# Performance work log

Hardware: AMD Instinct MI355X
Metric: run time of the kernel (lower is better)

The kernel has to match this reference:

```python
import jax, jax.numpy as jnp
import numpy as np

D_MODEL = 768
NUM_HEADS = 12
HEAD_DIM = D_MODEL // NUM_HEADS
LN_EPS = 1e-5
MASK_NEG = -1000000.0


def setup_inputs() -> dict:
    key = jax.random.key(0)
    ks = jax.random.split(key, 10)
    B, L, S = 2, 2048, 2048
    s = 1.0 / np.sqrt(D_MODEL)
    return {
        "q": jax.random.normal(ks[0], (B, L, D_MODEL), jnp.float32),
        "k": jax.random.normal(ks[1], (B, S, D_MODEL), jnp.float32),
        "v": jax.random.normal(ks[2], (B, S, D_MODEL), jnp.float32),
        "attention_mask": jnp.ones((B, S), jnp.int32),
        "Wq": jax.random.normal(ks[3], (D_MODEL, D_MODEL), jnp.float32) * s,
        "Wk": jax.random.normal(ks[4], (D_MODEL, D_MODEL), jnp.float32) * s,
        "Wv": jax.random.normal(ks[5], (D_MODEL, D_MODEL), jnp.float32) * s,
        "W": jax.random.normal(ks[6], (D_MODEL, D_MODEL), jnp.float32) * s,
        "b": jnp.zeros((D_MODEL,), jnp.float32),
        "gamma": jnp.ones((D_MODEL,), jnp.float32),
        "beta": jnp.zeros((D_MODEL,), jnp.float32),
    }


def reference(q, k, v, attention_mask, Wq, Wk, Wv, W, b, gamma, beta):
    B, L, D = q.shape
    S = k.shape[1]
    H, hd = NUM_HEADS, HEAD_DIM
    # projections (torch Linear: x @ W^T), split heads -> (B,H,L,hd)
    Q = (q @ Wq.T).reshape(B, L, H, hd).transpose(0, 2, 1, 3)
    K = (k @ Wk.T).reshape(B, S, H, hd).transpose(0, 2, 1, 3)
    V = (v @ Wv.T).reshape(B, S, H, hd).transpose(0, 2, 1, 3)
    # scores (B,H,L,S) with additive key-padding mask
    scores = jnp.einsum("bhld,bhsd->bhls", Q, K) / np.sqrt(hd)
    mask_score = (1.0 - attention_mask.astype(q.dtype))[:, None, None, :] * MASK_NEG
    att = jax.nn.softmax(scores + mask_score, axis=-1)  # dropout p=0 (eval)
    # attend, merge heads, output projection (with bias)
    O = jnp.einsum("bhls,bhsd->bhld", att, V).transpose(0, 2, 1, 3).reshape(B, L, D)
    O = O @ W.T + b  # state dropout p=0 (eval)
    # residual + LayerNorm
    x = q + O
    mu = jnp.mean(x, axis=-1, keepdims=True)
    var = jnp.mean(jnp.square(x - mu), axis=-1, keepdims=True)
    return (x - mu) * jax.lax.rsqrt(var + LN_EPS) * gamma + beta
```

## Files before the change

kernel.cpp:

```cpp
#include <hip/hip_runtime.h>
#include <hip/hip_bf16.h>
#include <math.h>


typedef unsigned short u16;
typedef unsigned int   u32;
typedef __bf16 bf16x8 __attribute__((ext_vector_type(8)));
typedef float  f32x4  __attribute__((ext_vector_type(4)));

#define DM   768
#define MR   4096
#define WSZ  589824

#define LOG2E 1.44269504089f
#define SM_C  15.0f
#define K1    (0.125f * LOG2E)

__device__ inline u16 bfbits(float f) {
    union { __bf16 b; u16 u; } x; x.b = (__bf16)f; return x.u;
}

__device__ inline uint4 cvt8(const float* src) {
    const float4* p = reinterpret_cast<const float4*>(src);
    float4 a = p[0], b = p[1];
    union { __bf16 h[8]; uint4 v; } u;
    u.h[0] = (__bf16)a.x; u.h[1] = (__bf16)a.y; u.h[2] = (__bf16)a.z; u.h[3] = (__bf16)a.w;
    u.h[4] = (__bf16)b.x; u.h[5] = (__bf16)b.y; u.h[6] = (__bf16)b.z; u.h[7] = (__bf16)b.w;
    return u.v;
}

__device__ inline uint4 cvt8v(float4 a, float4 b) {
    union { __bf16 h[8]; uint4 v; } u;
    u.h[0] = (__bf16)a.x; u.h[1] = (__bf16)a.y; u.h[2] = (__bf16)a.z; u.h[3] = (__bf16)a.w;
    u.h[4] = (__bf16)b.x; u.h[5] = (__bf16)b.y; u.h[6] = (__bf16)b.z; u.h[7] = (__bf16)b.w;
    return u.v;
}

__global__ __launch_bounds__(256) void wcvt(
    const float* __restrict__ w0, const float* __restrict__ w1,
    const float* __restrict__ w2, const float* __restrict__ w3,
    u16* __restrict__ dst)
{
    const float* src = (blockIdx.y == 0) ? w0 : (blockIdx.y == 1) ? w1
                     : (blockIdx.y == 2) ? w2 : w3;
    size_t idx = ((size_t)blockIdx.x * 256 + threadIdx.x) * 8;
    *reinterpret_cast<uint4*>(&dst[(size_t)blockIdx.y * WSZ + idx]) = cvt8(&src[idx]);
}

__global__ __launch_bounds__(256, 2) void gemm_qkv(
    const float* __restrict__ xq, const float* __restrict__ xk, const float* __restrict__ xv,
    const u16* __restrict__ Wb4,
    u16* __restrict__ oq, u16* __restrict__ ok, u16* __restrict__ ov)
{
    const int mode = blockIdx.z;
    const float* X = (mode == 0) ? xq : (mode == 1) ? xk : xv;
    const u16* Wb  = Wb4 + (size_t)mode * WSZ;
    u16* out       = (mode == 0) ? oq : (mode == 1) ? ok : ov;

    __shared__ __attribute__((aligned(16))) u16 As[2][64][72];
    __shared__ __attribute__((aligned(16))) u16 Bs[2][64][72];

    const int tid  = threadIdx.x;
    const int lane = tid & 63;
    const int w    = tid >> 6;
    const int wm   = (w >> 1) * 32;
    const int wn   = (w & 1) * 32;
    const int quad = lane >> 4;
    const int l16  = lane & 15;
    const int tm   = blockIdx.x * 64;
    const int tn   = blockIdx.y * 64;

    const int row0 = tid >> 3,         col0 = (tid & 7) * 8;
    const int row1 = (tid + 256) >> 3, col1 = ((tid + 256) & 7) * 8;

    const float* a0p = &X[(size_t)(tm + row0) * 768 + col0];
    const float* a1p = &X[(size_t)(tm + row1) * 768 + col1];
    const u16*   b0p = &Wb[(size_t)(tn + row0) * 768 + col0];
    const u16*   b1p = &Wb[(size_t)(tn + row1) * 768 + col1];

    f32x4 acc[2][2] = {};

    {
        *reinterpret_cast<uint4*>(&As[0][row0][col0]) = cvt8(a0p);
        *reinterpret_cast<uint4*>(&As[0][row1][col1]) = cvt8(a1p);
        *reinterpret_cast<uint4*>(&Bs[0][row0][col0]) = *reinterpret_cast<const uint4*>(b0p);
        *reinterpret_cast<uint4*>(&Bs[0][row1][col1]) = *reinterpret_cast<const uint4*>(b1p);
    }

    for (int kt = 0; kt < 12; kt++) {
        const int cur = kt & 1;
        __syncthreads();

        float4 af0a, af0b, af1a, af1b; uint4 bt0, bt1;
        if (kt < 11) {
            const int ko = (kt + 1) * 64;
            af0a = *reinterpret_cast<const float4*>(a0p + ko);
            af0b = *reinterpret_cast<const float4*>(a0p + ko + 4);
            af1a = *reinterpret_cast<const float4*>(a1p + ko);
            af1b = *reinterpret_cast<const float4*>(a1p + ko + 4);
            bt0  = *reinterpret_cast<const uint4*>(b0p + ko);
            bt1  = *reinterpret_cast<const uint4*>(b1p + ko);
        }

        #pragma unroll
        for (int kk = 0; kk < 2; kk++) {
            bf16x8 a0 = *reinterpret_cast<const bf16x8*>(&As[cur][wm + l16     ][kk*32 + quad*8]);
            bf16x8 a1 = *reinterpret_cast<const bf16x8*>(&As[cur][wm + 16 + l16][kk*32 + quad*8]);
            bf16x8 b0 = *reinterpret_cast<const bf16x8*>(&Bs[cur][wn + l16     ][kk*32 + quad*8]);
            bf16x8 b1 = *reinterpret_cast<const bf16x8*>(&Bs[cur][wn + 16 + l16][kk*32 + quad*8]);
            acc[0][0] = __builtin_amdgcn_mfma_f32_16x16x32_bf16(a0, b0, acc[0][0], 0, 0, 0);
            acc[0][1] = __builtin_amdgcn_mfma_f32_16x16x32_bf16(a0, b1, acc[0][1], 0, 0, 0);
            acc[1][0] = __builtin_amdgcn_mfma_f32_16x16x32_bf16(a1, b0, acc[1][0], 0, 0, 0);
            acc[1][1] = __builtin_amdgcn_mfma_f32_16x16x32_bf16(a1, b1, acc[1][1], 0, 0, 0);
        }

        if (kt < 11) {
            const int nxt = cur ^ 1;
            *reinterpret_cast<uint4*>(&As[nxt][row0][col0]) = cvt8v(af0a, af0b);
            *reinterpret_cast<uint4*>(&As[nxt][row1][col1]) = cvt8v(af1a, af1b);
            *reinterpret_cast<uint4*>(&Bs[nxt][row0][col0]) = bt0;
            *reinterpret_cast<uint4*>(&Bs[nxt][row1][col1]) = bt1;
        }
    }

    #pragma unroll
    for (int i = 0; i < 2; i++)
        #pragma unroll
        for (int j = 0; j < 2; j++)
            #pragma unroll
            for (int r = 0; r < 4; r++) {
                int gm = tm + wm + i * 16 + quad * 4 + r;
                int gn = tn + wn + j * 16 + l16;
                int b = gm >> 11, l = gm & 2047;
                int h = gn >> 6,  d = gn & 63;
                u16 bv = bfbits(acc[i][j][r]);
                if (mode == 2)
                    out[((size_t)(b * 12 + h) * 64 + d) * 2048 + l] = bv;
                else
                    out[((size_t)(b * 12 + h) * 2048 + l) * 64 + d] = bv;
            }
}

__global__ __launch_bounds__(256, 2) void gemm_out(
    const u16* __restrict__ Oa, const u16* __restrict__ Wb,
    const float* __restrict__ bias, const float* __restrict__ resid,
    float* __restrict__ Xb)
{
    __shared__ __attribute__((aligned(16))) u16 As[2][64][72];
    __shared__ __attribute__((aligned(16))) u16 Bs[2][64][72];

    const int tid  = threadIdx.x;
    const int lane = tid & 63;
    const int w    = tid >> 6;
    const int wm   = (w >> 1) * 32;
    const int wn   = (w & 1) * 32;
    const int quad = lane >> 4;
    const int l16  = lane & 15;
    const int tm   = blockIdx.x * 64;
    const int tn   = blockIdx.y * 64;

    const int row0 = tid >> 3,         col0 = (tid & 7) * 8;
    const int row1 = (tid + 256) >> 3, col1 = ((tid + 256) & 7) * 8;

    const u16* a0p = &Oa[(size_t)(tm + row0) * 768 + col0];
    const u16* a1p = &Oa[(size_t)(tm + row1) * 768 + col1];
    const u16* b0p = &Wb[(size_t)(tn + row0) * 768 + col0];
    const u16* b1p = &Wb[(size_t)(tn + row1) * 768 + col1];

    f32x4 acc[2][2] = {};

    {
        *reinterpret_cast<uint4*>(&As[0][row0][col0]) = *reinterpret_cast<const uint4*>(a0p);
        *reinterpret_cast<uint4*>(&As[0][row1][col1]) = *reinterpret_cast<const uint4*>(a1p);
        *reinterpret_cast<uint4*>(&Bs[0][row0][col0]) = *reinterpret_cast<const uint4*>(b0p);
        *reinterpret_cast<uint4*>(&Bs[0][row1][col1]) = *reinterpret_cast<const uint4*>(b1p);
    }

    for (int kt = 0; kt < 12; kt++) {
        const int cur = kt & 1;
        __syncthreads();

        uint4 at0, at1, bt0, bt1;
        if (kt < 11) {
            const int ko = (kt + 1) * 64;
            at0 = *reinterpret_cast<const uint4*>(a0p + ko);
            at1 = *reinterpret_cast<const uint4*>(a1p + ko);
            bt0 = *reinterpret_cast<const uint4*>(b0p + ko);
            bt1 = *reinterpret_cast<const uint4*>(b1p + ko);
        }

        #pragma unroll
        for (int kk = 0; kk < 2; kk++) {
            bf16x8 a0 = *reinterpret_cast<const bf16x8*>(&As[cur][wm + l16     ][kk*32 + quad*8]);
            bf16x8 a1 = *reinterpret_cast<const bf16x8*>(&As[cur][wm + 16 + l16][kk*32 + quad*8]);
            bf16x8 b0 = *reinterpret_cast<const bf16x8*>(&Bs[cur][wn + l16     ][kk*32 + quad*8]);
            bf16x8 b1 = *reinterpret_cast<const bf16x8*>(&Bs[cur][wn + 16 + l16][kk*32 + quad*8]);
            acc[0][0] = __builtin_amdgcn_mfma_f32_16x16x32_bf16(a0, b0, acc[0][0], 0, 0, 0);
            acc[0][1] = __builtin_amdgcn_mfma_f32_16x16x32_bf16(a0, b1, acc[0][1], 0, 0, 0);
            acc[1][0] = __builtin_amdgcn_mfma_f32_16x16x32_bf16(a1, b0, acc[1][0], 0, 0, 0);
            acc[1][1] = __builtin_amdgcn_mfma_f32_16x16x32_bf16(a1, b1, acc[1][1], 0, 0, 0);
        }

        if (kt < 11) {
            const int nxt = cur ^ 1;
            *reinterpret_cast<uint4*>(&As[nxt][row0][col0]) = at0;
            *reinterpret_cast<uint4*>(&As[nxt][row1][col1]) = at1;
            *reinterpret_cast<uint4*>(&Bs[nxt][row0][col0]) = bt0;
            *reinterpret_cast<uint4*>(&Bs[nxt][row1][col1]) = bt1;
        }
    }

    #pragma unroll
    for (int i = 0; i < 2; i++)
        #pragma unroll
        for (int j = 0; j < 2; j++)
            #pragma unroll
            for (int r = 0; r < 4; r++) {
                int gm = tm + wm + i * 16 + quad * 4 + r;
                int gn = tn + wn + j * 16 + l16;
                Xb[(size_t)gm * 768 + gn] = acc[i][j][r] + bias[gn] + resid[(size_t)gm * 768 + gn];
            }
}

__global__ __launch_bounds__(256, 3) void attn(
    const u16* __restrict__ Qp, const u16* __restrict__ Kp, const u16* __restrict__ Vt,
    const int* __restrict__ amask, u16* __restrict__ Oatt)
{
    __shared__ __attribute__((aligned(16))) unsigned char smem[4 * 64 * 40 * 2 + 2048 * 4];
    u16 (*Ps)[64][40] = reinterpret_cast<u16(*)[64][40]>(smem);
    float* maskC = reinterpret_cast<float*>(smem + 20480);
    float (*Obuf)[72] = reinterpret_cast<float(*)[72]>(smem);

    const int tid  = threadIdx.x;
    const int lane = tid & 63;
    const int w    = tid >> 6;
    const int quad = lane >> 4;
    const int l16  = lane & 15;
    const int qt = blockIdx.x;
    const int h  = blockIdx.y;
    const int b  = blockIdx.z;

    #pragma unroll
    for (int i = 0; i < 8; i++) {
        int s = tid + i * 256;
        maskC[s] = amask[b * 2048 + s] ? (-SM_C * LOG2E) : -2.0e6f;
    }
    __syncthreads();

    const u16* Qbase = Qp + ((size_t)(b * 12 + h) * 2048 + qt * 64) * 64;
    const u16* Kb2   = Kp + (size_t)(b * 12 + h) * 2048 * 64 + (size_t)w * 32 * 64;
    const u16* Vb2   = Vt + (size_t)(b * 12 + h) * 64 * 2048 + (size_t)w * 32;

    bf16x8 qfrag[4][2];
    #pragma unroll
    for (int qb = 0; qb < 4; qb++)
        #pragma unroll
        for (int kk = 0; kk < 2; kk++)
            qfrag[qb][kk] = *reinterpret_cast<const bf16x8*>(
                &Qbase[(qb * 16 + l16) * 64 + kk * 32 + quad * 8]);

    bf16x8 onesf = {};
    if (l16 == 0) {
        #pragma unroll
        for (int i = 0; i < 8; i++) onesf[i] = (__bf16)1.0f;
    }

    f32x4 oacc[4][4] = {};
    f32x4 sacc[4]    = {};

    for (int st = 0; st < 16; st++) {
        bf16x8 kf[2][2], vf[4];
        #pragma unroll
        for (int ct = 0; ct < 2; ct++)
            #pragma unroll
            for (int kk = 0; kk < 2; kk++)
                kf[ct][kk] = *reinterpret_cast<const bf16x8*>(
                    &Kb2[(size_t)(st * 128 + ct * 16 + l16) * 64 + kk * 32 + quad * 8]);
        #pragma unroll
        for (int cd = 0; cd < 4; cd++)
            vf[cd] = *reinterpret_cast<const bf16x8*>(
                &Vb2[(size_t)(cd * 16 + l16) * 2048 + st * 128 + quad * 8]);

        #pragma unroll
        for (int qb = 0; qb < 4; qb++)
            #pragma unroll
            for (int ct = 0; ct < 2; ct++) {
                f32x4 s = {};
                s = __builtin_amdgcn_mfma_f32_16x16x32_bf16(kf[ct][0], qfrag[qb][0], s, 0, 0, 0);
                s = __builtin_amdgcn_mfma_f32_16x16x32_bf16(kf[ct][1], qfrag[qb][1], s, 0, 0, 0);
                f32x4 cc = *reinterpret_cast<const f32x4*>(
                    &maskC[st * 128 + w * 32 + ct * 16 + quad * 4]);
                union { u16 h[4]; uint2 v2; } pk;
                #pragma unroll
                for (int r = 0; r < 4; r++)
                    pk.h[r] = bfbits(__builtin_amdgcn_exp2f(__builtin_fmaf(s[r], K1, cc[r])));
                *reinterpret_cast<uint2*>(&Ps[w][qb * 16 + l16][ct * 16 + quad * 4]) = pk.v2;
            }

        bf16x8 pf[4];
        #pragma unroll
        for (int qb = 0; qb < 4; qb++)
            pf[qb] = *reinterpret_cast<const bf16x8*>(&Ps[w][qb * 16 + l16][quad * 8]);
        #pragma unroll
        for (int qb = 0; qb < 4; qb++)
            sacc[qb] = __builtin_amdgcn_mfma_f32_16x16x32_bf16(pf[qb], onesf, sacc[qb], 0, 0, 0);
        #pragma unroll
        for (int qb = 0; qb < 4; qb++)
            #pragma unroll
            for (int cd = 0; cd < 4; cd++)
                oacc[qb][cd] = __builtin_amdgcn_mfma_f32_16x16x32_bf16(pf[qb], vf[cd], oacc[qb][cd], 0, 0, 0);
    }

    __syncthreads();
    for (int wv = 0; wv < 4; wv++) {
        if (w == wv) {
            #pragma unroll
            for (int qb = 0; qb < 4; qb++) {
                #pragma unroll
                for (int cd = 0; cd < 4; cd++)
                    #pragma unroll
                    for (int r = 0; r < 4; r++) {
                        float* cell = &Obuf[qb * 16 + quad * 4 + r][cd * 16 + l16];
                        if (wv == 0) *cell = oacc[qb][cd][r];
                        else         *cell += oacc[qb][cd][r];
                    }
                if (l16 == 0) {
                    #pragma unroll
                    for (int r = 0; r < 4; r++) {
                        float* cell = &Obuf[qb * 16 + quad * 4 + r][64];
                        if (wv == 0) *cell = sacc[qb][r];
                        else         *cell += sacc[qb][r];
                    }
                }
            }
        }
        __syncthreads();
    }

    #pragma unroll
    for (int g = 0; g < 4; g++) {
        int unit = tid + g * 256;
        int row = unit >> 4;
        int c4  = (unit & 15) * 4;
        float rinv = 1.0f / Obuf[row][64];
        union { u16 h[4]; uint2 v; } o;
        #pragma unroll
        for (int j = 0; j < 4; j++)
            o.h[j] = bfbits(Obuf[row][c4 + j] * rinv);
        *reinterpret_cast<uint2*>(
            &Oatt[(size_t)(b * 2048 + qt * 64 + row) * 768 + h * 64 + c4]) = o.v;
    }
}

__global__ __launch_bounds__(256) void ln_kernel(
    float* __restrict__ X, const float* __restrict__ gamma,
    const float* __restrict__ beta)
{
    const int row = blockIdx.x;
    const int tid = threadIdx.x;
    float* xr = X + (size_t)row * 768;

    float v[3], s = 0.f, s2 = 0.f;
    #pragma unroll
    for (int i = 0; i < 3; i++) {
        v[i] = xr[tid + i * 256];
        s += v[i];
        s2 += v[i] * v[i];
    }
    #pragma unroll
    for (int off = 32; off >= 1; off >>= 1) {
        s  += __shfl_xor(s,  off, 64);
        s2 += __shfl_xor(s2, off, 64);
    }
    __shared__ float rs[4], rs2[4];
    int w = tid >> 6, lane = tid & 63;
    if (lane == 0) { rs[w] = s; rs2[w] = s2; }
    __syncthreads();
    s  = rs[0] + rs[1] + rs[2] + rs[3];
    s2 = rs2[0] + rs2[1] + rs2[2] + rs2[3];
    float mu = s * (1.0f / 768.0f);
    float var = s2 * (1.0f / 768.0f) - mu * mu;
    float rstd = rsqrtf(var + 1e-5f);
    #pragma unroll
    for (int i = 0; i < 3; i++) {
        int c = tid + i * 256;
        xr[c] = (v[i] - mu) * rstd * gamma[c] + beta[c];
    }
}

extern "C" void kernel_launch(void* const* d_in, const int* in_sizes, int n_in,
                              void* d_out, int out_size, void* d_ws, size_t ws_size,
                              hipStream_t stream)
{
    const float* q   = (const float*)d_in[0];
    const float* k   = (const float*)d_in[1];
    const float* v   = (const float*)d_in[2];
    const int*   am  = (const int*)d_in[3];
    const float* Wq  = (const float*)d_in[4];
    const float* Wk  = (const float*)d_in[5];
    const float* Wv  = (const float*)d_in[6];
    const float* W   = (const float*)d_in[7];
    const float* bb  = (const float*)d_in[8];
    const float* gam = (const float*)d_in[9];
    const float* bet = (const float*)d_in[10];

    u16* Wb4 = (u16*)d_ws;
    u16* Qp  = Wb4 + (size_t)4 * WSZ;
    u16* Kp  = Qp + (size_t)MR * DM;
    u16* Vt  = Kp + (size_t)MR * DM;
    u16* Oa  = Vt + (size_t)MR * DM;
    float* Xb = (float*)d_out;

    wcvt<<<dim3(288, 4), 256, 0, stream>>>(Wq, Wk, Wv, W, Wb4);
    gemm_qkv<<<dim3(64, 12, 3), 256, 0, stream>>>(q, k, v, Wb4, Qp, Kp, Vt);
    attn<<<dim3(32, 12, 2), 256, 0, stream>>>(Qp, Kp, Vt, am, Oa);
    gemm_out<<<dim3(64, 12), 256, 0, stream>>>(Oa, Wb4 + (size_t)3 * WSZ, bb, q, Xb);
    ln_kernel<<<4096, 256, 0, stream>>>(Xb, gam, bet);
}
```

Baseline: 218.1 us.

## Shrink attention query tile, prefetch K/V fragments, precompute mask globally

The attention kernel now handles 32 query rows per block instead of 64, doubling the grid and raising the occupancy hint from 3 to 4 blocks per CU. K and V fragments for the next key tile are loaded as soon as the current ones are consumed, a one-step software prefetch. The key-padding mask is precomputed once into a float buffer by an extra block in the weight-conversion kernel, which removes per-block LDS mask setup. The cross-wave reduction of partial outputs now uses two LDS buffers in two stages instead of four serial rounds. The trade-off is that each block redoes the full K/V stream for half as many queries, doubling K/V load traffic.

```diff
diff --git a/kernel.cpp b/kernel.cpp
--- a/kernel.cpp
+++ b/kernel.cpp
@@ -39,8 +39,20 @@
 __global__ __launch_bounds__(256) void wcvt(
     const float* __restrict__ w0, const float* __restrict__ w1,
     const float* __restrict__ w2, const float* __restrict__ w3,
-    u16* __restrict__ dst)
-{
+    const int* __restrict__ am, u16* __restrict__ dst,
+    float* __restrict__ maskF)
+{
+    if (blockIdx.x == 288) {
+        int i = (blockIdx.y * 256 + threadIdx.x) * 4;
+        int4 m = *reinterpret_cast<const int4*>(&am[i]);
+        float4 o;
+        o.x = m.x ? (-SM_C * LOG2E) : -2.0e6f;
+        o.y = m.y ? (-SM_C * LOG2E) : -2.0e6f;
+        o.z = m.z ? (-SM_C * LOG2E) : -2.0e6f;
+        o.w = m.w ? (-SM_C * LOG2E) : -2.0e6f;
+        *reinterpret_cast<float4*>(&maskF[i]) = o;
+        return;
+    }
     const float* src = (blockIdx.y == 0) ? w0 : (blockIdx.y == 1) ? w1
                      : (blockIdx.y == 2) ? w2 : w3;
     size_t idx = ((size_t)blockIdx.x * 256 + threadIdx.x) * 8;
@@ -222,14 +234,14 @@
             }
 }
 
-__global__ __launch_bounds__(256, 3) void attn(
+__global__ __launch_bounds__(256, 4) void attn(
     const u16* __restrict__ Qp, const u16* __restrict__ Kp, const u16* __restrict__ Vt,
-    const int* __restrict__ amask, u16* __restrict__ Oatt)
-{
-    __shared__ __attribute__((aligned(16))) unsigned char smem[4 * 64 * 40 * 2 + 2048 * 4];
-    u16 (*Ps)[64][40] = reinterpret_cast<u16(*)[64][40]>(smem);
-    float* maskC = reinterpret_cast<float*>(smem + 20480);
-    float (*Obuf)[72] = reinterpret_cast<float(*)[72]>(smem);
+    const float* __restrict__ maskF, u16* __restrict__ Oatt)
+{
+    __shared__ __attribute__((aligned(16))) unsigned char smem[2 * 32 * 68 * 4];
+    u16 (*Ps)[32][40] = reinterpret_cast<u16(*)[32][40]>(smem);
+    float (*O0)[68] = reinterpret_cast<float(*)[68]>(smem);
+    float (*O1)[68] = reinterpret_cast<float(*)[68]>(smem + 32 * 68 * 4);
 
     const int tid  = threadIdx.x;
     const int lane = tid & 63;
@@ -240,20 +252,14 @@
     const int h  = blockIdx.y;
     const int b  = blockIdx.z;
 
-    #pragma unroll
-    for (int i = 0; i < 8; i++) {
-        int s = tid + i * 256;
-        maskC[s] = amask[b * 2048 + s] ? (-SM_C * LOG2E) : -2.0e6f;
-    }
-    __syncthreads();
-
-    const u16* Qbase = Qp + ((size_t)(b * 12 + h) * 2048 + qt * 64) * 64;
+    const u16* Qbase = Qp + ((size_t)(b * 12 + h) * 2048 + qt * 32) * 64;
     const u16* Kb2   = Kp + (size_t)(b * 12 + h) * 2048 * 64 + (size_t)w * 32 * 64;
     const u16* Vb2   = Vt + (size_t)(b * 12 + h) * 64 * 2048 + (size_t)w * 32;
-
-    bf16x8 qfrag[4][2];
-    #pragma unroll
-    for (int qb = 0; qb < 4; qb++)
+    const float* mB  = maskF + b * 2048 + w * 32;
+
+    bf16x8 qfrag[2][2];
+    #pragma unroll
+    for (int qb = 0; qb < 2; qb++)
         #pragma unroll
         for (int kk = 0; kk < 2; kk++)
             qfrag[qb][kk] = *reinterpret_cast<const bf16x8*>(
@@ -265,90 +271,120 @@
         for (int i = 0; i < 8; i++) onesf[i] = (__bf16)1.0f;
     }
 
-    f32x4 oacc[4][4] = {};
-    f32x4 sacc[4]    = {};
+    f32x4 oacc[2][4] = {};
+    f32x4 sacc[2]    = {};
+
+    bf16x8 kf[2][2], vf[4];
+    #pragma unroll
+    for (int ct = 0; ct < 2; ct++)
+        #pragma unroll
+        for (int kk = 0; kk < 2; kk++)
+            kf[ct][kk] = *reinterpret_cast<const bf16x8*>(
+                &Kb2[(size_t)(ct * 16 + l16) * 64 + kk * 32 + quad * 8]);
+    #pragma unroll
+    for (int cd = 0; cd < 4; cd++)
+        vf[cd] = *reinterpret_cast<const bf16x8*>(
+            &Vb2[(size_t)(cd * 16 + l16) * 2048 + quad * 8]);
 
     for (int st = 0; st < 16; st++) {
-        bf16x8 kf[2][2], vf[4];
-        #pragma unroll
-        for (int ct = 0; ct < 2; ct++)
-            #pragma unroll
-            for (int kk = 0; kk < 2; kk++)
-                kf[ct][kk] = *reinterpret_cast<const bf16x8*>(
-                    &Kb2[(size_t)(st * 128 + ct * 16 + l16) * 64 + kk * 32 + quad * 8]);
-        #pragma unroll
-        for (int cd = 0; cd < 4; cd++)
-            vf[cd] = *reinterpret_cast<const bf16x8*>(
-                &Vb2[(size_t)(cd * 16 + l16) * 2048 + st * 128 + quad * 8]);
-
-        #pragma unroll
-        for (int qb = 0; qb < 4; qb++)
-            #pragma unroll
-            for (int ct = 0; ct < 2; ct++) {
+        const int stn = (st + 1) & 15;
+
+        #pragma unroll
+        for (int ct = 0; ct < 2; ct++) {
+            f32x4 sv[2];
+            #pragma unroll
+            for (int qb = 0; qb < 2; qb++) {
                 f32x4 s = {};
                 s = __builtin_amdgcn_mfma_f32_16x16x32_bf16(kf[ct][0], qfrag[qb][0], s, 0, 0, 0);
                 s = __builtin_amdgcn_mfma_f32_16x16x32_bf16(kf[ct][1], qfrag[qb][1], s, 0, 0, 0);
-                f32x4 cc = *reinterpret_cast<const f32x4*>(
-                    &maskC[st * 128 + w * 32 + ct * 16 + quad * 4]);
+                sv[qb] = s;
+            }
+            #pragma unroll
+            for (int kk = 0; kk < 2; kk++)
+                kf[ct][kk] = *reinterpret_cast<const bf16x8*>(
+                    &Kb2[(size_t)(stn * 128 + ct * 16 + l16) * 64 + kk * 32 + quad * 8]);
+
+            f32x4 cc = *reinterpret_cast<const f32x4*>(&mB[st * 128 + ct * 16 + quad * 4]);
+            #pragma unroll
+            for (int qb = 0; qb < 2; qb++) {
                 union { u16 h[4]; uint2 v2; } pk;
                 #pragma unroll
                 for (int r = 0; r < 4; r++)
-                    pk.h[r] = bfbits(__builtin_amdgcn_exp2f(__builtin_fmaf(s[r], K1, cc[r])));
+                    pk.h[r] = bfbits(__builtin_amdgcn_exp2f(__builtin_fmaf(sv[qb][r], K1, cc[r])));
                 *reinterpret_cast<uint2*>(&Ps[w][qb * 16 + l16][ct * 16 + quad * 4]) = pk.v2;
             }
-
-        bf16x8 pf[4];
-        #pragma unroll
-        for (int qb = 0; qb < 4; qb++)
+        }
+
+        bf16x8 pf[2];
+        #pragma unroll
+        for (int qb = 0; qb < 2; qb++)
             pf[qb] = *reinterpret_cast<const bf16x8*>(&Ps[w][qb * 16 + l16][quad * 8]);
         #pragma unroll
-        for (int qb = 0; qb < 4; qb++)
+        for (int qb = 0; qb < 2; qb++)
             sacc[qb] = __builtin_amdgcn_mfma_f32_16x16x32_bf16(pf[qb], onesf, sacc[qb], 0, 0, 0);
         #pragma unroll
-        for (int qb = 0; qb < 4; qb++)
+        for (int qb = 0; qb < 2; qb++)
             #pragma unroll
             for (int cd = 0; cd < 4; cd++)
                 oacc[qb][cd] = __builtin_amdgcn_mfma_f32_16x16x32_bf16(pf[qb], vf[cd], oacc[qb][cd], 0, 0, 0);
+
+        #pragma unroll
+        for (int cd = 0; cd < 4; cd++)
+            vf[cd] = *reinterpret_cast<const bf16x8*>(
+                &Vb2[(size_t)(cd * 16 + l16) * 2048 + stn * 128 + quad * 8]);
     }
 
     __syncthreads();
-    for (int wv = 0; wv < 4; wv++) {
-        if (w == wv) {
-            #pragma unroll
-            for (int qb = 0; qb < 4; qb++) {
+    float (*Ob)[68] = (w & 1) ? O1 : O0;
+    if (w >= 2) {
+        #pragma unroll
+        for (int qb = 0; qb < 2; qb++) {
+            #pragma unroll
+            for (int cd = 0; cd < 4; cd++)
                 #pragma unroll
-                for (int cd = 0; cd < 4; cd++)
-                    #pragma unroll
-                    for (int r = 0; r < 4; r++) {
-                        float* cell = &Obuf[qb * 16 + quad * 4 + r][cd * 16 + l16];
-                        if (wv == 0) *cell = oacc[qb][cd][r];
-                        else         *cell += oacc[qb][cd][r];
-                    }
-                if (l16 == 0) {
-                    #pragma unroll
-                    for (int r = 0; r < 4; r++) {
-                        float* cell = &Obuf[qb * 16 + quad * 4 + r][64];
-                        if (wv == 0) *cell = sacc[qb][r];
-                        else         *cell += sacc[qb][r];
-                    }
+                for (int r = 0; r < 4; r++)
+                    Ob[qb * 16 + quad * 4 + r][cd * 16 + l16] = oacc[qb][cd][r];
+            if (l16 == 0) {
+                #pragma unroll
+                for (int r = 0; r < 4; r++)
+                    Ob[qb * 16 + quad * 4 + r][64] = sacc[qb][r];
+            }
+        }
+    }
+    __syncthreads();
+    if (w < 2) {
+        #pragma unroll
+        for (int qb = 0; qb < 2; qb++) {
+            #pragma unroll
+            for (int cd = 0; cd < 4; cd++)
+                #pragma unroll
+                for (int r = 0; r < 4; r++) {
+                    float* c = &Ob[qb * 16 + quad * 4 + r][cd * 16 + l16];
+                    *c += oacc[qb][cd][r];
                 }
-            }
-        }
-        __syncthreads();
-    }
-
-    #pragma unroll
-    for (int g = 0; g < 4; g++) {
+            if (l16 == 0) {
+                #pragma unroll
+                for (int r = 0; r < 4; r++) {
+                    float* c = &Ob[qb * 16 + quad * 4 + r][64];
+                    *c += sacc[qb][r];
+                }
+            }
+        }
+    }
+    __syncthreads();
+
+    #pragma unroll
+    for (int g = 0; g < 2; g++) {
         int unit = tid + g * 256;
         int row = unit >> 4;
         int c4  = (unit & 15) * 4;
-        float rinv = 1.0f / Obuf[row][64];
+        float rinv = 1.0f / (O0[row][64] + O1[row][64]);
         union { u16 h[4]; uint2 v; } o;
         #pragma unroll
         for (int j = 0; j < 4; j++)
-            o.h[j] = bfbits(Obuf[row][c4 + j] * rinv);
+            o.h[j] = bfbits((O0[row][c4 + j] + O1[row][c4 + j]) * rinv);
         *reinterpret_cast<uint2*>(
-            &Oatt[(size_t)(b * 2048 + qt * 64 + row) * 768 + h * 64 + c4]) = o.v;
+            &Oatt[(size_t)(b * 2048 + qt * 32 + row) * 768 + h * 64 + c4]) = o.v;
     }
 }
 
@@ -409,11 +445,12 @@
     u16* Kp  = Qp + (size_t)MR * DM;
     u16* Vt  = Kp + (size_t)MR * DM;
     u16* Oa  = Vt + (size_t)MR * DM;
+    float* maskF = (float*)(Oa + (size_t)MR * DM);
     float* Xb = (float*)d_out;
 
-    wcvt<<<dim3(288, 4), 256, 0, stream>>>(Wq, Wk, Wv, W, Wb4);
+    wcvt<<<dim3(289, 4), 256, 0, stream>>>(Wq, Wk, Wv, W, am, Wb4, maskF);
     gemm_qkv<<<dim3(64, 12, 3), 256, 0, stream>>>(q, k, v, Wb4, Qp, Kp, Vt);
-    attn<<<dim3(32, 12, 2), 256, 0, stream>>>(Qp, Kp, Vt, am, Oa);
+    attn<<<dim3(64, 12, 2), 256, 0, stream>>>(Qp, Kp, Vt, maskF, Oa);
     gemm_out<<<dim3(64, 12), 256, 0, stream>>>(Oa, Wb4 + (size_t)3 * WSZ, bb, q, Xb);
     ln_kernel<<<4096, 256, 0, stream>>>(Xb, gam, bet);
 }
```

Measured after the change: 261.8 us. +20.1%, slower.

## Prefetch K/V fragments across attention steps, precompute mask, remap blocks

Applied to the files above, without the earlier changes.

Converts the attention key-padding mask to float once in the weight-conversion kernel and reads it from global memory, which drops the per-block shared-memory mask setup and its barrier and shrinks LDS use. K and V fragments for the next step are loaded during the current step so global-load latency overlaps the MFMA and exp work, and s_setprio raises wave priority around the MFMA bursts. The grid is flattened to 1D and remapped so groups of 8 consecutive blocks cover different head/batch pairs, which changes how K/V traffic spreads across L2 and cache partitions. The extra prefetch registers may reduce occupancy, and the last iteration prefetches wrapped data it never uses.

```diff
diff --git a/kernel.cpp b/kernel.cpp
--- a/kernel.cpp
+++ b/kernel.cpp
@@ -39,8 +39,20 @@
 __global__ __launch_bounds__(256) void wcvt(
     const float* __restrict__ w0, const float* __restrict__ w1,
     const float* __restrict__ w2, const float* __restrict__ w3,
-    u16* __restrict__ dst)
-{
+    const int* __restrict__ am, u16* __restrict__ dst,
+    float* __restrict__ maskF)
+{
+    if (blockIdx.x == 288) {
+        int i = (blockIdx.y * 256 + threadIdx.x) * 4;
+        int4 m = *reinterpret_cast<const int4*>(&am[i]);
+        float4 o;
+        o.x = m.x ? (-SM_C * LOG2E) : -2.0e6f;
+        o.y = m.y ? (-SM_C * LOG2E) : -2.0e6f;
+        o.z = m.z ? (-SM_C * LOG2E) : -2.0e6f;
+        o.w = m.w ? (-SM_C * LOG2E) : -2.0e6f;
+        *reinterpret_cast<float4*>(&maskF[i]) = o;
+        return;
+    }
     const float* src = (blockIdx.y == 0) ? w0 : (blockIdx.y == 1) ? w1
                      : (blockIdx.y == 2) ? w2 : w3;
     size_t idx = ((size_t)blockIdx.x * 256 + threadIdx.x) * 8;
@@ -224,32 +236,30 @@
 
 __global__ __launch_bounds__(256, 3) void attn(
     const u16* __restrict__ Qp, const u16* __restrict__ Kp, const u16* __restrict__ Vt,
-    const int* __restrict__ amask, u16* __restrict__ Oatt)
-{
-    __shared__ __attribute__((aligned(16))) unsigned char smem[4 * 64 * 40 * 2 + 2048 * 4];
+    const float* __restrict__ maskF, u16* __restrict__ Oatt)
+{
+    __shared__ __attribute__((aligned(16))) unsigned char smem[4 * 64 * 40 * 2];
     u16 (*Ps)[64][40] = reinterpret_cast<u16(*)[64][40]>(smem);
-    float* maskC = reinterpret_cast<float*>(smem + 20480);
-    float (*Obuf)[72] = reinterpret_cast<float(*)[72]>(smem);
+    float (*Obuf)[68] = reinterpret_cast<float(*)[68]>(smem);
 
     const int tid  = threadIdx.x;
     const int lane = tid & 63;
     const int w    = tid >> 6;
     const int quad = lane >> 4;
     const int l16  = lane & 15;
-    const int qt = blockIdx.x;
-    const int h  = blockIdx.y;
-    const int b  = blockIdx.z;
-
-    #pragma unroll
-    for (int i = 0; i < 8; i++) {
-        int s = tid + i * 256;
-        maskC[s] = amask[b * 2048 + s] ? (-SM_C * LOG2E) : -2.0e6f;
-    }
-    __syncthreads();
+
+    const int bi  = blockIdx.x;
+    const int c   = bi & 7;
+    const int k8  = bi >> 3;
+    const int qt  = k8 & 31;
+    const int hc  = c + 8 * (k8 >> 5);
+    const int h   = hc % 12;
+    const int b   = hc / 12;
 
     const u16* Qbase = Qp + ((size_t)(b * 12 + h) * 2048 + qt * 64) * 64;
     const u16* Kb2   = Kp + (size_t)(b * 12 + h) * 2048 * 64 + (size_t)w * 32 * 64;
     const u16* Vb2   = Vt + (size_t)(b * 12 + h) * 64 * 2048 + (size_t)w * 32;
+    const float* mB  = maskF + b * 2048 + w * 32;
 
     bf16x8 qfrag[4][2];
     #pragma unroll
@@ -268,39 +278,54 @@
     f32x4 oacc[4][4] = {};
     f32x4 sacc[4]    = {};
 
+    bf16x8 kf[2][2], vf[4];
+    #pragma unroll
+    for (int ct = 0; ct < 2; ct++)
+        #pragma unroll
+        for (int kk = 0; kk < 2; kk++)
+            kf[ct][kk] = *reinterpret_cast<const bf16x8*>(
+                &Kb2[(size_t)(ct * 16 + l16) * 64 + kk * 32 + quad * 8]);
+    #pragma unroll
+    for (int cd = 0; cd < 4; cd++)
+        vf[cd] = *reinterpret_cast<const bf16x8*>(
+            &Vb2[(size_t)(cd * 16 + l16) * 2048 + quad * 8]);
+
     for (int st = 0; st < 16; st++) {
-        bf16x8 kf[2][2], vf[4];
-        #pragma unroll
-        for (int ct = 0; ct < 2; ct++)
-            #pragma unroll
-            for (int kk = 0; kk < 2; kk++)
-                kf[ct][kk] = *reinterpret_cast<const bf16x8*>(
-                    &Kb2[(size_t)(st * 128 + ct * 16 + l16) * 64 + kk * 32 + quad * 8]);
-        #pragma unroll
-        for (int cd = 0; cd < 4; cd++)
-            vf[cd] = *reinterpret_cast<const bf16x8*>(
-                &Vb2[(size_t)(cd * 16 + l16) * 2048 + st * 128 + quad * 8]);
-
-        #pragma unroll
-        for (int qb = 0; qb < 4; qb++)
-            #pragma unroll
-            for (int ct = 0; ct < 2; ct++) {
+        const int stn = (st + 1) & 15;
+
+        #pragma unroll
+        for (int ct = 0; ct < 2; ct++) {
+            f32x4 sv[4];
+            __builtin_amdgcn_s_setprio(1);
+            #pragma unroll
+            for (int qb = 0; qb < 4; qb++) {
                 f32x4 s = {};
                 s = __builtin_amdgcn_mfma_f32_16x16x32_bf16(kf[ct][0], qfrag[qb][0], s, 0, 0, 0);
                 s = __builtin_amdgcn_mfma_f32_16x16x32_bf16(kf[ct][1], qfrag[qb][1], s, 0, 0, 0);
-                f32x4 cc = *reinterpret_cast<const f32x4*>(
-                    &maskC[st * 128 + w * 32 + ct * 16 + quad * 4]);
+                sv[qb] = s;
+            }
+            __builtin_amdgcn_s_setprio(0);
+            #pragma unroll
+            for (int kk = 0; kk < 2; kk++)
+                kf[ct][kk] = *reinterpret_cast<const bf16x8*>(
+                    &Kb2[(size_t)(stn * 128 + ct * 16 + l16) * 64 + kk * 32 + quad * 8]);
+
+            f32x4 cc = *reinterpret_cast<const f32x4*>(&mB[st * 128 + ct * 16 + quad * 4]);
+            #pragma unroll
+            for (int qb = 0; qb < 4; qb++) {
                 union { u16 h[4]; uint2 v2; } pk;
                 #pragma unroll
                 for (int r = 0; r < 4; r++)
-                    pk.h[r] = bfbits(__builtin_amdgcn_exp2f(__builtin_fmaf(s[r], K1, cc[r])));
+                    pk.h[r] = bfbits(__builtin_amdgcn_exp2f(__builtin_fmaf(sv[qb][r], K1, cc[r])));
                 *reinterpret_cast<uint2*>(&Ps[w][qb * 16 + l16][ct * 16 + quad * 4]) = pk.v2;
             }
+        }
 
         bf16x8 pf[4];
         #pragma unroll
         for (int qb = 0; qb < 4; qb++)
             pf[qb] = *reinterpret_cast<const bf16x8*>(&Ps[w][qb * 16 + l16][quad * 8]);
+        __builtin_amdgcn_s_setprio(1);
         #pragma unroll
         for (int qb = 0; qb < 4; qb++)
             sacc[qb] = __builtin_amdgcn_mfma_f32_16x16x32_bf16(pf[qb], onesf, sacc[qb], 0, 0, 0);
@@ -309,6 +334,12 @@
             #pragma unroll
             for (int cd = 0; cd < 4; cd++)
                 oacc[qb][cd] = __builtin_amdgcn_mfma_f32_16x16x32_bf16(pf[qb], vf[cd], oacc[qb][cd], 0, 0, 0);
+        __builtin_amdgcn_s_setprio(0);
+
+        #pragma unroll
+        for (int cd = 0; cd < 4; cd++)
+            vf[cd] = *reinterpret_cast<const bf16x8*>(
+                &Vb2[(size_t)(cd * 16 + l16) * 2048 + stn * 128 + quad * 8]);
     }
 
     __syncthreads();
@@ -409,11 +440,12 @@
     u16* Kp  = Qp + (size_t)MR * DM;
     u16* Vt  = Kp + (size_t)MR * DM;
     u16* Oa  = Vt + (size_t)MR * DM;
+    float* maskF = (float*)(Oa + (size_t)MR * DM);
     float* Xb = (float*)d_out;
 
-    wcvt<<<dim3(288, 4), 256, 0, stream>>>(Wq, Wk, Wv, W, Wb4);
+    wcvt<<<dim3(289, 4), 256, 0, stream>>>(Wq, Wk, Wv, W, am, Wb4, maskF);
     gemm_qkv<<<dim3(64, 12, 3), 256, 0, stream>>>(q, k, v, Wb4, Qp, Kp, Vt);
-    attn<<<dim3(32, 12, 2), 256, 0, stream>>>(Qp, Kp, Vt, am, Oa);
+    attn<<<dim3(768), 256, 0, stream>>>(Qp, Kp, Vt, maskF, Oa);
     gemm_out<<<dim3(64, 12), 256, 0, stream>>>(Oa, Wb4 + (size_t)3 * WSZ, bb, q, Xb);
     ln_kernel<<<4096, 256, 0, stream>>>(Xb, gam, bet);
 }
```

Result: slower. 281.2 us (+29.0%).

## Enlarge GEMM tiles to 128x128 and load B tiles via global_load_lds

Applied to the files above, without the earlier changes.

Both projection GEMMs move from 64x64 to 128x128 block tiles, with each wave computing a 64x64 sub-tile of 4x4 MFMAs, which raises operand reuse per LDS load. Bf16 tiles are now copied straight from global memory into LDS with global_load_lds, skipping registers. The double-buffered LDS pipeline is replaced by a single buffer with register prefetch for A in the QKV GEMM only, so B-load latency is no longer overlapped. Grids shrink to 576 and 192 blocks, which cuts parallelism, and the unpadded 64-wide LDS rows may cause bank conflicts.

```diff
diff --git a/kernel.cpp b/kernel.cpp
--- a/kernel.cpp
+++ b/kernel.cpp
@@ -36,6 +36,12 @@
     return u.v;
 }
 
+typedef __attribute__((address_space(3))) unsigned int lds_u32;
+typedef __attribute__((address_space(1))) const unsigned int glb_u32;
+__device__ inline void gload16(const u16* g, u16* l) {
+    __builtin_amdgcn_global_load_lds((glb_u32*)g, (lds_u32*)l, 16, 0, 0);
+}
+
 __global__ __launch_bounds__(256) void wcvt(
     const float* __restrict__ w0, const float* __restrict__ w1,
     const float* __restrict__ w2, const float* __restrict__ w3,
@@ -57,80 +63,80 @@
     const u16* Wb  = Wb4 + (size_t)mode * WSZ;
     u16* out       = (mode == 0) ? oq : (mode == 1) ? ok : ov;
 
-    __shared__ __attribute__((aligned(16))) u16 As[2][64][72];
-    __shared__ __attribute__((aligned(16))) u16 Bs[2][64][72];
+    __shared__ __attribute__((aligned(16))) u16 As[128][72];
+    __shared__ __attribute__((aligned(16))) u16 Bs[128][64];
 
     const int tid  = threadIdx.x;
     const int lane = tid & 63;
     const int w    = tid >> 6;
-    const int wm   = (w >> 1) * 32;
-    const int wn   = (w & 1) * 32;
+    const int wr   = (w >> 1) * 64;
+    const int wc   = (w & 1) * 64;
     const int quad = lane >> 4;
     const int l16  = lane & 15;
-    const int tm   = blockIdx.x * 64;
-    const int tn   = blockIdx.y * 64;
-
-    const int row0 = tid >> 3,         col0 = (tid & 7) * 8;
-    const int row1 = (tid + 256) >> 3, col1 = ((tid + 256) & 7) * 8;
-
-    const float* a0p = &X[(size_t)(tm + row0) * 768 + col0];
-    const float* a1p = &X[(size_t)(tm + row1) * 768 + col1];
-    const u16*   b0p = &Wb[(size_t)(tn + row0) * 768 + col0];
-    const u16*   b1p = &Wb[(size_t)(tn + row1) * 768 + col1];
-
-    f32x4 acc[2][2] = {};
-
-    {
-        *reinterpret_cast<uint4*>(&As[0][row0][col0]) = cvt8(a0p);
-        *reinterpret_cast<uint4*>(&As[0][row1][col1]) = cvt8(a1p);
-        *reinterpret_cast<uint4*>(&Bs[0][row0][col0]) = *reinterpret_cast<const uint4*>(b0p);
-        *reinterpret_cast<uint4*>(&Bs[0][row1][col1]) = *reinterpret_cast<const uint4*>(b1p);
-    }
+    const int tm   = blockIdx.x * 128;
+    const int tn   = blockIdx.y * 128;
+
+    const int arow = tid >> 1;
+    const int ach  = (tid & 1) * 32;
+    const float* Ap = &X[(size_t)(tm + arow) * 768 + ach];
+
+    const int brow = w * 32 + (lane >> 3);
+    const int bcol = (lane & 7) * 8;
+    const u16* Bp = &Wb[(size_t)(tn + brow) * 768 + bcol];
+
+    f32x4 acc[4][4] = {};
+    float4 aPre[8];
+
+    #pragma unroll
+    for (int q = 0; q < 8; q++)
+        aPre[q] = *reinterpret_cast<const float4*>(Ap + q * 4);
 
     for (int kt = 0; kt < 12; kt++) {
-        const int cur = kt & 1;
+        const int k0 = kt * 64;
+        if (kt) __syncthreads();
+
+        *reinterpret_cast<uint4*>(&As[arow][ach +  0]) = cvt8v(aPre[0], aPre[1]);
+        *reinterpret_cast<uint4*>(&As[arow][ach +  8]) = cvt8v(aPre[2], aPre[3]);
+        *reinterpret_cast<uint4*>(&As[arow][ach + 16]) = cvt8v(aPre[4], aPre[5]);
+        *reinterpret_cast<uint4*>(&As[arow][ach + 24]) = cvt8v(aPre[6], aPre[7]);
+
+        #pragma unroll
+        for (int j = 0; j < 4; j++)
+            gload16(Bp + (size_t)j * 8 * 768 + k0, &Bs[w * 32 + j * 8][0]);
+
         __syncthreads();
 
-        float4 af0a, af0b, af1a, af1b; uint4 bt0, bt1;
         if (kt < 11) {
-            const int ko = (kt + 1) * 64;
-            af0a = *reinterpret_cast<const float4*>(a0p + ko);
-            af0b = *reinterpret_cast<const float4*>(a0p + ko + 4);
-            af1a = *reinterpret_cast<const float4*>(a1p + ko);
-            af1b = *reinterpret_cast<const float4*>(a1p + ko + 4);
-            bt0  = *reinterpret_cast<const uint4*>(b0p + ko);
-            bt1  = *reinterpret_cast<const uint4*>(b1p + ko);
+            #pragma unroll
+            for (int q = 0; q < 8; q++)
+                aPre[q] = *reinterpret_cast<const float4*>(Ap + k0 + 64 + q * 4);
         }
 
         #pragma unroll
         for (int kk = 0; kk < 2; kk++) {
-            bf16x8 a0 = *reinterpret_cast<const bf16x8*>(&As[cur][wm + l16     ][kk*32 + quad*8]);
-            bf16x8 a1 = *reinterpret_cast<const bf16x8*>(&As[cur][wm + 16 + l16][kk*32 + quad*8]);
-            bf16x8 b0 = *reinterpret_cast<const bf16x8*>(&Bs[cur][wn + l16     ][kk*32 + quad*8]);
-            bf16x8 b1 = *reinterpret_cast<const bf16x8*>(&Bs[cur][wn + 16 + l16][kk*32 + quad*8]);
-            acc[0][0] = __builtin_amdgcn_mfma_f32_16x16x32_bf16(a0, b0, acc[0][0], 0, 0, 0);
-            acc[0][1] = __builtin_amdgcn_mfma_f32_16x16x32_bf16(a0, b1, acc[0][1], 0, 0, 0);
-            acc[1][0] = __builtin_amdgcn_mfma_f32_16x16x32_bf16(a1, b0, acc[1][0], 0, 0, 0);
-            acc[1][1] = __builtin_amdgcn_mfma_f32_16x16x32_bf16(a1, b1, acc[1][1], 0, 0, 0);
+            bf16x8 av[4], bv[4];
+            #pragma unroll
+            for (int i = 0; i < 4; i++)
+                av[i] = *reinterpret_cast<const bf16x8*>(&As[wr + i * 16 + l16][kk * 32 + quad * 8]);
+            #pragma unroll
+            for (int j = 0; j < 4; j++)
+                bv[j] = *reinterpret_cast<const bf16x8*>(&Bs[wc + j * 16 + l16][kk * 32 + quad * 8]);
+            #pragma unroll
+            for (int i = 0; i < 4; i++)
+                #pragma unroll
+                for (int j = 0; j < 4; j++)
+                    acc[i][j] = __builtin_amdgcn_mfma_f32_16x16x32_bf16(av[i], bv[j], acc[i][j], 0, 0, 0);
         }
-
-        if (kt < 11) {
-            const int nxt = cur ^ 1;
-            *reinterpret_cast<uint4*>(&As[nxt][row0][col0]) = cvt8v(af0a, af0b);
-            *reinterpret_cast<uint4*>(&As[nxt][row1][col1]) = cvt8v(af1a, af1b);
-            *reinterpret_cast<uint4*>(&Bs[nxt][row0][col0]) = bt0;
-            *reinterpret_cast<uint4*>(&Bs[nxt][row1][col1]) = bt1;
-        }
-    }
-
-    #pragma unroll
-    for (int i = 0; i < 2; i++)
-        #pragma unroll
-        for (int j = 0; j < 2; j++)
+    }
+
+    #pragma unroll
+    for (int i = 0; i < 4; i++)
+        #pragma unroll
+        for (int j = 0; j < 4; j++)
             #pragma unroll
             for (int r = 0; r < 4; r++) {
-                int gm = tm + wm + i * 16 + quad * 4 + r;
-                int gn = tn + wn + j * 16 + l16;
+                int gm = tm + wr + i * 16 + quad * 4 + r;
+                int gn = tn + wc + j * 16 + l16;
                 int b = gm >> 11, l = gm & 2047;
                 int h = gn >> 6,  d = gn & 63;
                 u16 bv = bfbits(acc[i][j][r]);
@@ -146,78 +152,63 @@
     const float* __restrict__ bias, const float* __restrict__ resid,
     float* __restrict__ Xb)
 {
-    __shared__ __attribute__((aligned(16))) u16 As[2][64][72];
-    __shared__ __attribute__((aligned(16))) u16 Bs[2][64][72];
+    __shared__ __attribute__((aligned(16))) u16 As[128][64];
+    __shared__ __attribute__((aligned(16))) u16 Bs[128][64];
 
     const int tid  = threadIdx.x;
     const int lane = tid & 63;
     const int w    = tid >> 6;
-    const int wm   = (w >> 1) * 32;
-    const int wn   = (w & 1) * 32;
+    const int wr   = (w >> 1) * 64;
+    const int wc   = (w & 1) * 64;
     const int quad = lane >> 4;
     const int l16  = lane & 15;
-    const int tm   = blockIdx.x * 64;
-    const int tn   = blockIdx.y * 64;
-
-    const int row0 = tid >> 3,         col0 = (tid & 7) * 8;
-    const int row1 = (tid + 256) >> 3, col1 = ((tid + 256) & 7) * 8;
-
-    const u16* a0p = &Oa[(size_t)(tm + row0) * 768 + col0];
-    const u16* a1p = &Oa[(size_t)(tm + row1) * 768 + col1];
-    const u16* b0p = &Wb[(size_t)(tn + row0) * 768 + col0];
-    const u16* b1p = &Wb[(size_t)(tn + row1) * 768 + col1];
-
-    f32x4 acc[2][2] = {};
-
-    {
-        *reinterpret_cast<uint4*>(&As[0][row0][col0]) = *reinterpret_cast<const uint4*>(a0p);
-        *reinterpret_cast<uint4*>(&As[0][row1][col1]) = *reinterpret_cast<const uint4*>(a1p);
-        *reinterpret_cast<uint4*>(&Bs[0][row0][col0]) = *reinterpret_cast<const uint4*>(b0p);
-        *reinterpret_cast<uint4*>(&Bs[0][row1][col1]) = *reinterpret_cast<const uint4*>(b1p);
-    }
+    const int tm   = blockIdx.x * 128;
+    const int tn   = blockIdx.y * 128;
+
+    const int srow = w * 32 + (lane >> 3);
+    const int scol = (lane & 7) * 8;
+    const u16* Apg = &Oa[(size_t)(tm + srow) * 768 + scol];
+    const u16* Bpg = &Wb[(size_t)(tn + srow) * 768 + scol];
+
+    f32x4 acc[4][4] = {};
 
     for (int kt = 0; kt < 12; kt++) {
-        const int cur = kt & 1;
+        const int k0 = kt * 64;
+        if (kt) __syncthreads();
+
+        #pragma unroll
+        for (int j = 0; j < 4; j++) {
+            gload16(Apg + (size_t)j * 8 * 768 + k0, &As[w * 32 + j * 8][0]);
+            gload16(Bpg + (size_t)j * 8 * 768 + k0, &Bs[w * 32 + j * 8][0]);
+        }
+
         __syncthreads();
 
-        uint4 at0, at1, bt0, bt1;
-        if (kt < 11) {
-            const int ko = (kt + 1) * 64;
-            at0 = *reinterpret_cast<const uint4*>(a0p + ko);
-            at1 = *reinterpret_cast<const uint4*>(a1p + ko);
-            bt0 = *reinterpret_cast<const uint4*>(b0p + ko);
-            bt1 = *reinterpret_cast<const uint4*>(b1p + ko);
+        #pragma unroll
+        for (int kk = 0; kk < 2; kk++) {
+            bf16x8 av[4], bv[4];
+            #pragma unroll
+            for (int i = 0; i < 4; i++)
+                av[i] = *reinterpret_cast<const bf16x8*>(&As[wr + i * 16 + l16][kk * 32 + quad * 8]);
+            #pragma unroll
+            for (int j = 0; j < 4; j++)
+                bv[j] = *reinterpret_cast<const bf16x8*>(&Bs[wc + j * 16 + l16][kk * 32 + quad * 8]);
+            #pragma unroll
+            for (int i = 0; i < 4; i++)
+                #pragma unroll
+                for (int j = 0; j < 4; j++)
+                    acc[i][j] = __builtin_amdgcn_mfma_f32_16x16x32_bf16(av[i], bv[j], acc[i][j], 0, 0, 0);
         }
-
-        #pragma unroll
-        for (int kk = 0; kk < 2; kk++) {
-            bf16x8 a0 = *reinterpret_cast<const bf16x8*>(&As[cur][wm + l16     ][kk*32 + quad*8]);
-            bf16x8 a1 = *reinterpret_cast<const bf16x8*>(&As[cur][wm + 16 + l16][kk*32 + quad*8]);
-            bf16x8 b0 = *reinterpret_cast<const bf16x8*>(&Bs[cur][wn + l16     ][kk*32 + quad*8]);
-            bf16x8 b1 = *reinterpret_cast<const bf16x8*>(&Bs[cur][wn + 16 + l16][kk*32 + quad*8]);
-            acc[0][0] = __builtin_amdgcn_mfma_f32_16x16x32_bf16(a0, b0, acc[0][0], 0, 0, 0);
-            acc[0][1] = __builtin_amdgcn_mfma_f32_16x16x32_bf16(a0, b1, acc[0][1], 0, 0, 0);
-            acc[1][0] = __builtin_amdgcn_mfma_f32_16x16x32_bf16(a1, b0, acc[1][0], 0, 0, 0);
-            acc[1][1] = __builtin_amdgcn_mfma_f32_16x16x32_bf16(a1, b1, acc[1][1], 0, 0, 0);
-        }
-
-        if (kt < 11) {
-            const int nxt = cur ^ 1;
-            *reinterpret_cast<uint4*>(&As[nxt][row0][col0]) = at0;
-            *reinterpret_cast<uint4*>(&As[nxt][row1][col1]) = at1;
-            *reinterpret_cast<uint4*>(&Bs[nxt][row0][col0]) = bt0;
-            *reinterpret_cast<uint4*>(&Bs[nxt][row1][col1]) = bt1;
-        }
-    }
-
-    #pragma unroll
-    for (int i = 0; i < 2; i++)
-        #pragma unroll
-        for (int j = 0; j < 2; j++)
+    }
+
+    #pragma unroll
+    for (int i = 0; i < 4; i++)
+        #pragma unroll
+        for (int j = 0; j < 4; j++)
             #pragma unroll
             for (int r = 0; r < 4; r++) {
-                int gm = tm + wm + i * 16 + quad * 4 + r;
-                int gn = tn + wn + j * 16 + l16;
+                int gm = tm + wr + i * 16 + quad * 4 + r;
+                int gn = tn + wc + j * 16 + l16;
                 Xb[(size_t)gm * 768 + gn] = acc[i][j][r] + bias[gn] + resid[(size_t)gm * 768 + gn];
             }
 }
@@ -412,8 +403,8 @@
     float* Xb = (float*)d_out;
 
     wcvt<<<dim3(288, 4), 256, 0, stream>>>(Wq, Wk, Wv, W, Wb4);
-    gemm_qkv<<<dim3(64, 12, 3), 256, 0, stream>>>(q, k, v, Wb4, Qp, Kp, Vt);
+    gemm_qkv<<<dim3(32, 6, 3), 256, 0, stream>>>(q, k, v, Wb4, Qp, Kp, Vt);
     attn<<<dim3(32, 12, 2), 256, 0, stream>>>(Qp, Kp, Vt, am, Oa);
-    gemm_out<<<dim3(64, 12), 256, 0, stream>>>(Oa, Wb4 + (size_t)3 * WSZ, bb, q, Xb);
+    gemm_out<<<dim3(32, 6), 256, 0, stream>>>(Oa, Wb4 + (size_t)3 * WSZ, bb, q, Xb);
     ln_kernel<<<4096, 256, 0, stream>>>(Xb, gam, bet);
 }
```

Result: slower. 234.8 us (+7.7%).
